# Kernel optimization log

Measured on AMD Instinct MI355X. Metric: run time of the kernel, lower is better.

The kernel has to match this reference:

```python
import jax, jax.numpy as jnp
import numpy as np

SHIFT = 1  # torch module picks +/-1 randomly at init; fixed to +1 for determinism


def setup_inputs() -> dict:
    key = jax.random.key(0)
    k1, k2 = jax.random.split(key)
    x = jax.random.normal(k1, (1, 512, 14, 14), dtype=jnp.float32)
    w = jax.random.normal(k2, (256, 256, 3), dtype=jnp.float32)
    return {"x": x, "w": w}


def reference(x, w):
    # (1,512,14,14) -> (1, o=2, i=256, H=14, W=14)
    t = x.reshape(1, 2, 256, 14, 14)
    # roll along W by +1 (torch.roll dim 4)
    t = jnp.roll(t, SHIFT, axis=4)
    # unfold(kernel=(3,1), padding=(1,0)) over the W axis after the
    # (1,7168,14,1) collapse == zero-padded 3-tap sliding windows along W.
    p = jnp.pad(t, ((0, 0), (0, 0), (0, 0), (0, 0), (1, 1)))
    # taps: (1,2,256,14,3,14) == (l,o,i,n,j,m) of the torch reshape
    taps = jnp.stack([p[..., 0:14], p[..., 1:15], p[..., 2:16]], axis=4)
    # 3-tap conv1d along W: contract input channel i and tap j
    out = jnp.einsum('loinjm,ikj->loknm', taps, w)  # (1,2,256,14,14)
    out = out.reshape(1, 512, 14, 14)
    # final roll along H (torch dim 2 of (1,512,14,14))
    out = jnp.roll(out, SHIFT, axis=2)
    return out
```

## Files before the change

### kernel.cpp

```cpp
#include <hip/hip_runtime.h>


#define BT 512

__global__ __launch_bounds__(BT) void shiftconv_kernel(
    const float* __restrict__ x,
    const float* __restrict__ w,
    float* __restrict__ out)
{
    __shared__ __align__(16) float smem[32 * 28 * 17 + 2];
    float* xs   = smem;
    float* part = smem;

    const int kt = blockIdx.x;
    const int h  = blockIdx.y;
    const int o  = blockIdx.z;
    const int t  = threadIdx.x;
    const int n  = (h + 13) % 14;

    xs[(t >> 1) * 16 + (t & 1) * 15] = 0.0f;
    for (int e = t; e < 256 * 14; e += BT) {
        int i  = e / 14;
        int ww = e - i * 14;
        float v = x[((size_t)(o * 256 + i) * 14 + n) * 14 + ww];
        xs[i * 16 + ((ww <= 12) ? (ww + 2) : 1)] = v;
    }
    __syncthreads();

    const int kk2 = t & 15;
    const int s   = t >> 4;
    const int kg0 = kt * 32 + 2 * kk2;
    const int i0  = s * 8;

    const float* wp = w + ((size_t)i0 * 256 + kg0) * 3;
    const float* xp = xs + i0 * 16;

    float accA[14], accB[14];
#pragma unroll
    for (int m = 0; m < 14; ++m) { accA[m] = 0.f; accB[m] = 0.f; }

#pragma unroll
    for (int i = 0; i < 8; ++i) {
        float4 q0 = *reinterpret_cast<const float4*>(xp);
        float4 q1 = *reinterpret_cast<const float4*>(xp + 4);
        float4 q2 = *reinterpret_cast<const float4*>(xp + 8);
        float4 q3 = *reinterpret_cast<const float4*>(xp + 12);
        float r[16] = {q0.x,q0.y,q0.z,q0.w, q1.x,q1.y,q1.z,q1.w,
                       q2.x,q2.y,q2.z,q2.w, q3.x,q3.y,q3.z,q3.w};
        float3 wa = *reinterpret_cast<const float3*>(wp);
        float3 wb = *reinterpret_cast<const float3*>(wp + 3);
#pragma unroll
        for (int m = 0; m < 14; ++m) {
            accA[m] = fmaf(r[m],   wa.x, accA[m]);
            accA[m] = fmaf(r[m+1], wa.y, accA[m]);
            accA[m] = fmaf(r[m+2], wa.z, accA[m]);
            accB[m] = fmaf(r[m],   wb.x, accB[m]);
            accB[m] = fmaf(r[m+1], wb.y, accB[m]);
            accB[m] = fmaf(r[m+2], wb.z, accB[m]);
        }
        xp += 16;
        wp += 768;
    }

    __syncthreads();

#pragma unroll
    for (int m = 0; m < 14; ++m) {
        part[(s * 28 + m)      * 17 + kk2] = accA[m];
        part[(s * 28 + 14 + m) * 17 + kk2] = accB[m];
    }
    __syncthreads();

    if (t < 448) {
        int kk = t & 31;
        int m  = t >> 5;
        int k2 = kk >> 1;
        int mu = (kk & 1) * 14 + m;
        float sum = 0.f;
#pragma unroll
        for (int si = 0; si < 32; ++si)
            sum += part[(si * 28 + mu) * 17 + k2];
        out[((size_t)(o * 256 + kt * 32 + kk) * 14 + h) * 14 + m] = sum;
    }
}

extern "C" void kernel_launch(void* const* d_in, const int* in_sizes, int n_in,
                              void* d_out, int out_size, void* d_ws, size_t ws_size,
                              hipStream_t stream) {
    const float* x = (const float*)d_in[0];
    const float* w = (const float*)d_in[1];
    float* out = (float*)d_out;

    dim3 grid(8, 14, 2);
    dim3 block(BT);
    shiftconv_kernel<<<grid, block, 0, stream>>>(x, w, out);
}
```

Before: 60.33 us.

## Prefetch inputs and weights into registers, swizzle shared tiles, transpose partial-sum layout

All x loads and all per-thread weights are issued into registers before the shared-memory stores and barrier, so global latency overlaps instead of being serialized with compute. Shared x rows are XOR-swizzled per 8-row group to reduce bank conflicts on the float4 reads. The partial-sum buffer is transposed so each output thread reads a contiguous row, and the reduction is split over four independent accumulators. This raises register pressure (48 weight floats plus 7 prefetched values) and changes the float summation order.

```diff
diff --git a/kernel.cpp b/kernel.cpp
--- a/kernel.cpp
+++ b/kernel.cpp
@@ -8,7 +8,7 @@
     const float* __restrict__ w,
     float* __restrict__ out)
 {
-    __shared__ __align__(16) float smem[32 * 28 * 17 + 2];
+    __shared__ __align__(16) float smem[448 * 33];
     float* xs   = smem;
     float* part = smem;
 
@@ -18,69 +18,95 @@
     const int t  = threadIdx.x;
     const int n  = (h + 13) % 14;
 
-    xs[(t >> 1) * 16 + (t & 1) * 15] = 0.0f;
-    for (int e = t; e < 256 * 14; e += BT) {
-        int i  = e / 14;
-        int ww = e - i * 14;
-        float v = x[((size_t)(o * 256 + i) * 14 + n) * 14 + ww];
-        xs[i * 16 + ((ww <= 12) ? (ww + 2) : 1)] = v;
-    }
-    __syncthreads();
-
     const int kk2 = t & 15;
     const int s   = t >> 4;
     const int kg0 = kt * 32 + 2 * kk2;
     const int i0  = s * 8;
+    const int sq  = s & 3;
+
+    float xv[7];
+#pragma unroll
+    for (int r = 0; r < 7; ++r) {
+        int e  = t + r * BT;
+        int i  = e / 14;
+        int ww = e - i * 14;
+        xv[r] = x[((size_t)(o * 256 + i) * 14 + n) * 14 + ww];
+    }
 
     const float* wp = w + ((size_t)i0 * 256 + kg0) * 3;
-    const float* xp = xs + i0 * 16;
+    float3 wa[8], wb[8];
+#pragma unroll
+    for (int i = 0; i < 8; ++i) {
+        wa[i] = *reinterpret_cast<const float3*>(wp);
+        wb[i] = *reinterpret_cast<const float3*>(wp + 3);
+        wp += 768;
+    }
+
+    {
+        int rz = t >> 1;
+        int cz = (t & 1) * 15;
+        xs[rz * 16 + (cz ^ (((rz >> 3) & 3) << 2))] = 0.0f;
+    }
+#pragma unroll
+    for (int r = 0; r < 7; ++r) {
+        int e  = t + r * BT;
+        int i  = e / 14;
+        int ww = e - i * 14;
+        int c  = (ww <= 12) ? (ww + 2) : 1;
+        xs[i * 16 + (c ^ (((i >> 3) & 3) << 2))] = xv[r];
+    }
+    __syncthreads();
 
     float accA[14], accB[14];
 #pragma unroll
     for (int m = 0; m < 14; ++m) { accA[m] = 0.f; accB[m] = 0.f; }
 
+    const float* xp = xs + i0 * 16;
 #pragma unroll
     for (int i = 0; i < 8; ++i) {
-        float4 q0 = *reinterpret_cast<const float4*>(xp);
-        float4 q1 = *reinterpret_cast<const float4*>(xp + 4);
-        float4 q2 = *reinterpret_cast<const float4*>(xp + 8);
-        float4 q3 = *reinterpret_cast<const float4*>(xp + 12);
-        float r[16] = {q0.x,q0.y,q0.z,q0.w, q1.x,q1.y,q1.z,q1.w,
-                       q2.x,q2.y,q2.z,q2.w, q3.x,q3.y,q3.z,q3.w};
-        float3 wa = *reinterpret_cast<const float3*>(wp);
-        float3 wb = *reinterpret_cast<const float3*>(wp + 3);
+        float r[16];
+#pragma unroll
+        for (int j = 0; j < 4; ++j) {
+            float4 q = *reinterpret_cast<const float4*>(xp + ((j ^ sq) << 2));
+            r[4 * j + 0] = q.x; r[4 * j + 1] = q.y;
+            r[4 * j + 2] = q.z; r[4 * j + 3] = q.w;
+        }
 #pragma unroll
         for (int m = 0; m < 14; ++m) {
-            accA[m] = fmaf(r[m],   wa.x, accA[m]);
-            accA[m] = fmaf(r[m+1], wa.y, accA[m]);
-            accA[m] = fmaf(r[m+2], wa.z, accA[m]);
-            accB[m] = fmaf(r[m],   wb.x, accB[m]);
-            accB[m] = fmaf(r[m+1], wb.y, accB[m]);
-            accB[m] = fmaf(r[m+2], wb.z, accB[m]);
+            accA[m] = fmaf(r[m],     wa[i].x, accA[m]);
+            accA[m] = fmaf(r[m + 1], wa[i].y, accA[m]);
+            accA[m] = fmaf(r[m + 2], wa[i].z, accA[m]);
+            accB[m] = fmaf(r[m],     wb[i].x, accB[m]);
+            accB[m] = fmaf(r[m + 1], wb[i].y, accB[m]);
+            accB[m] = fmaf(r[m + 2], wb[i].z, accB[m]);
         }
         xp += 16;
-        wp += 768;
     }
 
     __syncthreads();
 
+    const int oA = (2 * kk2) * 14;
+    const int oB = oA + 14;
 #pragma unroll
     for (int m = 0; m < 14; ++m) {
-        part[(s * 28 + m)      * 17 + kk2] = accA[m];
-        part[(s * 28 + 14 + m) * 17 + kk2] = accB[m];
+        part[(oA + m) * 33 + s] = accA[m];
+        part[(oB + m) * 33 + s] = accB[m];
     }
     __syncthreads();
 
     if (t < 448) {
-        int kk = t & 31;
-        int m  = t >> 5;
-        int k2 = kk >> 1;
-        int mu = (kk & 1) * 14 + m;
-        float sum = 0.f;
+        float s0 = 0.f, s1 = 0.f, s2 = 0.f, s3 = 0.f;
+        const float* pr = part + t * 33;
 #pragma unroll
-        for (int si = 0; si < 32; ++si)
-            sum += part[(si * 28 + mu) * 17 + k2];
-        out[((size_t)(o * 256 + kt * 32 + kk) * 14 + h) * 14 + m] = sum;
+        for (int si = 0; si < 32; si += 4) {
+            s0 += pr[si + 0];
+            s1 += pr[si + 1];
+            s2 += pr[si + 2];
+            s3 += pr[si + 3];
+        }
+        int u = t / 14;
+        int m = t - u * 14;
+        out[((size_t)(o * 256 + kt * 32 + u) * 14 + h) * 14 + m] = (s0 + s1) + (s2 + s3);
     }
 }
 
```

Result: faster. 58.97 us (-2.3%).
